# Optimization experiments

Measured on AMD Instinct MI355X. Metric: run time of the kernel, lower is better.

Reference implementation:

```python
import jax, jax.numpy as jnp
import numpy as np

N1, N2, K = 262144, 65536, 16   # dense points, coarse points, knn neighbors
CIN, COUT = 64, 64              # in_planes, out_planes
EPS = 1e-5


def bn(x, g, b, m, v):
    # eval-mode BatchNorm1d with learned affine and running stats
    return (x - m) * jax.lax.rsqrt(v + EPS) * g + b


def setup_inputs() -> dict:
    key = jax.random.key(0)
    ks = jax.random.split(key, 32)
    u = lambda k, *s: jax.random.normal(k, s, jnp.float32)
    lin = lambda k, o, i: jax.random.normal(k, (o, i), jnp.float32) / np.float32(np.sqrt(i))
    inp = dict(
        p1=u(ks[0], N1, 3), p2=u(ks[1], N2, 3),
        x1=u(ks[2], N1, COUT), x2=u(ks[3], N2, CIN),
        knn_idx=jax.random.randint(ks[4], (N2, K), 0, N1),
        # linear1: Linear(COUT,COUT) + BN + ReLU
        w1=lin(ks[5], COUT, COUT), b1=0.01 * u(ks[6], COUT),
        g1=jnp.ones(COUT), be1=jnp.zeros(COUT),
        m1=0.1 * u(ks[7], COUT), v1=jax.random.uniform(ks[8], (COUT,), minval=0.5, maxval=1.5),
        # linear2: Linear(CIN,COUT) + BN + ReLU
        w2=lin(ks[9], COUT, CIN), b2=0.01 * u(ks[10], COUT),
        g2=jnp.ones(COUT), be2=jnp.zeros(COUT),
        m2=0.1 * u(ks[11], COUT), v2=jax.random.uniform(ks[12], (COUT,), minval=0.5, maxval=1.5),
        # channel_shrinker: Linear(CIN+3,CIN) + BN + ReLU + Linear(CIN,1)
        ws1=lin(ks[13], CIN, CIN + 3), bs1=0.01 * u(ks[14], CIN),
        gs=jnp.ones(CIN), bes=jnp.zeros(CIN),
        ms=0.1 * u(ks[15], CIN), vs=jax.random.uniform(ks[16], (CIN,), minval=0.5, maxval=1.5),
        ws2=lin(ks[17], 1, CIN), bs2=0.01 * u(ks[18], 1),
    )
    return inp


def reference(p1, p2, x1, x2, knn_idx,
              w1, b1, g1, be1, m1, v1,
              w2, b2, g2, be2, m2, v2,
              ws1, bs1, gs, bes, ms, vs, ws2, bs2):
    idx = knn_idx.reshape(-1)                                   # [M] = [N2*K], indices into p1
    # relative position of each knn neighbor to its coarse query point
    p_r = p1[idx].reshape(N2, K, 3) - p2[:, None, :]            # [N2,K,3]
    x2k = jnp.concatenate(
        [p_r, jnp.broadcast_to(x2[:, None, :], (N2, K, CIN))], axis=-1
    ).reshape(N2 * K, CIN + 3)                                  # [M, CIN+3]
    # channel_shrinker MLP -> scalar logit per (coarse, neighbor) pair
    h = jax.nn.relu(bn(x2k @ ws1.T + bs1, gs, bes, ms, vs))     # [M, CIN]
    logit = (h @ ws2.T + bs2)[:, 0]                             # [M]
    # scatter_softmax over variable in-degree groups keyed by dense point idx
    gmax = jax.lax.stop_gradient(jax.ops.segment_max(logit, idx, num_segments=N1))
    e = jnp.exp(logit - gmax[idx])
    denom = jax.ops.segment_sum(e, idx, num_segments=N1)
    prob = e / denom[idx]                                       # [M]
    # linear2(x2), broadcast over K neighbors, weight, scatter-sum to dense points
    up_feat = jax.nn.relu(bn(x2 @ w2.T + b2, g2, be2, m2, v2))  # [N2, COUT]
    weighted = (up_feat[:, None, :] * prob.reshape(N2, K, 1)).reshape(N2 * K, COUT)
    up = jax.ops.segment_sum(weighted, idx, num_segments=N1)    # [N1, COUT]
    # skip branch: linear1(x1)
    y1 = jax.nn.relu(bn(x1 @ w1.T + b1, g1, be1, m1, v1))       # [N1, COUT]
    return y1 + up
```

## Files before the change

kernel.cpp:

```cpp
#include <hip/hip_runtime.h>

#define CN1 262144
#define CN2 65536
#define CK  16
#define CM  (CN2*CK)

typedef unsigned short u16;
typedef unsigned int   u32;
typedef float f32x4 __attribute__((ext_vector_type(4)));

__device__ __forceinline__ float b2f(u16 h) {
    union { u32 u; float f; } v; v.u = ((u32)h) << 16; return v.f;
}
__device__ __forceinline__ u16 f2b(float f) {
    union { float f; u32 u; } v; v.f = f;
    u32 lsb = (v.u >> 16) & 1u;
    return (u16)((v.u + 0x7FFFu + lsb) >> 16);
}
__device__ __forceinline__ float u2f(u32 u) {
    union { u32 u; float f; } v; v.u = u; return v.f;
}
__device__ __forceinline__ u32 f2u(float f) {
    union { float f; u32 u; } v; v.f = f; return v.u;
}

#define W_POS   0
#define W_FT    256
#define W_AS    12544
#define W_BS    12608
#define W_WS2   12672
#define W_A2    12736
#define W_B2    12800
#define W_A1    12864
#define W_B1    12928
#define W_BS2   12992
#define W_MODE  13000
#define W_W1T   13056
#define W_W2T   17152
#define W_JP    21248

__device__ __forceinline__ float ldv(const void* p, size_t i, int bf) {
    return bf ? b2f(((const u16*)p)[i]) : ((const float*)p)[i];
}

#define FMA4(A, Wv) \
    (A).x = fmaf(xv_, (Wv).x, (A).x); (A).y = fmaf(xv_, (Wv).y, (A).y); \
    (A).z = fmaf(xv_, (Wv).z, (A).z); (A).w = fmaf(xv_, (Wv).w, (A).w);

#define DECL_ACC16 \
    f32x4 A0={0,0,0,0},A1={0,0,0,0},A2={0,0,0,0},A3={0,0,0,0}, \
          A4={0,0,0,0},A5={0,0,0,0},A6={0,0,0,0},A7={0,0,0,0}, \
          A8={0,0,0,0},A9={0,0,0,0},A10={0,0,0,0},A11={0,0,0,0}, \
          A12={0,0,0,0},A13={0,0,0,0},A14={0,0,0,0},A15={0,0,0,0};

#define WSTEP16(wt, ivar, xval) { \
    float xv_ = (xval); \
    const f32x4* wr_ = (const f32x4*)((wt) + ((size_t)(ivar) << 6)); \
    FMA4(A0, wr_[0])   FMA4(A1, wr_[1])   FMA4(A2, wr_[2])   FMA4(A3, wr_[3]) \
    FMA4(A4, wr_[4])   FMA4(A5, wr_[5])   FMA4(A6, wr_[6])   FMA4(A7, wr_[7]) \
    FMA4(A8, wr_[8])   FMA4(A9, wr_[9])   FMA4(A10,wr_[10])  FMA4(A11,wr_[11]) \
    FMA4(A12,wr_[12])  FMA4(A13,wr_[13])  FMA4(A14,wr_[14])  FMA4(A15,wr_[15]) }

#define GEMV64T(bf, xrow_f, xrow_u4, wt) \
    if (bf) { \
        const uint4* xu_ = (xrow_u4); \
        _Pragma("unroll 2") \
        for (int ii_ = 0; ii_ < 8; ++ii_) { \
            uint4 xc_ = xu_[ii_]; \
            WSTEP16(wt, ii_*8+0, b2f((u16)(xc_.x & 0xffffu))) \
            WSTEP16(wt, ii_*8+1, b2f((u16)(xc_.x >> 16))) \
            WSTEP16(wt, ii_*8+2, b2f((u16)(xc_.y & 0xffffu))) \
            WSTEP16(wt, ii_*8+3, b2f((u16)(xc_.y >> 16))) \
            WSTEP16(wt, ii_*8+4, b2f((u16)(xc_.z & 0xffffu))) \
            WSTEP16(wt, ii_*8+5, b2f((u16)(xc_.z >> 16))) \
            WSTEP16(wt, ii_*8+6, b2f((u16)(xc_.w & 0xffffu))) \
            WSTEP16(wt, ii_*8+7, b2f((u16)(xc_.w >> 16))) \
        } \
    } else { \
        const float4* xf_ = (xrow_f); \
        _Pragma("unroll 2") \
        for (int ii_ = 0; ii_ < 8; ++ii_) { \
            float4 xa_ = xf_[2*ii_], xb_ = xf_[2*ii_+1]; \
            WSTEP16(wt, ii_*8+0, xa_.x) WSTEP16(wt, ii_*8+1, xa_.y) \
            WSTEP16(wt, ii_*8+2, xa_.z) WSTEP16(wt, ii_*8+3, xa_.w) \
            WSTEP16(wt, ii_*8+4, xb_.x) WSTEP16(wt, ii_*8+5, xb_.y) \
            WSTEP16(wt, ii_*8+6, xb_.z) WSTEP16(wt, ii_*8+7, xb_.w) \
        } \
    }

#define DECL_ACC8 \
    f32x4 A0={0,0,0,0},A1={0,0,0,0},A2={0,0,0,0},A3={0,0,0,0}, \
          A4={0,0,0,0},A5={0,0,0,0},A6={0,0,0,0},A7={0,0,0,0};

#define WSTEP8(wtco, ivar, xval) { \
    float xv_ = (xval); \
    const f32x4* wr_ = (const f32x4*)((wtco) + ((size_t)(ivar) << 6)); \
    FMA4(A0, wr_[0])  FMA4(A1, wr_[1])  FMA4(A2, wr_[2])  FMA4(A3, wr_[3]) \
    FMA4(A4, wr_[4])  FMA4(A5, wr_[5])  FMA4(A6, wr_[6])  FMA4(A7, wr_[7]) }

#define GEMV32T(bf, xrow_f, xrow_u4, wtco) \
    if (bf) { \
        const uint4* xu_ = (xrow_u4); \
        _Pragma("unroll 2") \
        for (int ii_ = 0; ii_ < 8; ++ii_) { \
            uint4 xc_ = xu_[ii_]; \
            WSTEP8(wtco, ii_*8+0, b2f((u16)(xc_.x & 0xffffu))) \
            WSTEP8(wtco, ii_*8+1, b2f((u16)(xc_.x >> 16))) \
            WSTEP8(wtco, ii_*8+2, b2f((u16)(xc_.y & 0xffffu))) \
            WSTEP8(wtco, ii_*8+3, b2f((u16)(xc_.y >> 16))) \
            WSTEP8(wtco, ii_*8+4, b2f((u16)(xc_.z & 0xffffu))) \
            WSTEP8(wtco, ii_*8+5, b2f((u16)(xc_.z >> 16))) \
            WSTEP8(wtco, ii_*8+6, b2f((u16)(xc_.w & 0xffffu))) \
            WSTEP8(wtco, ii_*8+7, b2f((u16)(xc_.w >> 16))) \
        } \
    } else { \
        const float4* xf_ = (xrow_f); \
        _Pragma("unroll 2") \
        for (int ii_ = 0; ii_ < 8; ++ii_) { \
            float4 xa_ = xf_[2*ii_], xb_ = xf_[2*ii_+1]; \
            WSTEP8(wtco, ii_*8+0, xa_.x) WSTEP8(wtco, ii_*8+1, xa_.y) \
            WSTEP8(wtco, ii_*8+2, xa_.z) WSTEP8(wtco, ii_*8+3, xa_.w) \
            WSTEP8(wtco, ii_*8+4, xb_.x) WSTEP8(wtco, ii_*8+5, xb_.y) \
            WSTEP8(wtco, ii_*8+6, xb_.z) WSTEP8(wtco, ii_*8+7, xb_.w) \
        } \
    }

#define BNR1(A, av, bv) \
    (A).x = fmaxf(fmaf((A).x,(av).x,(bv).x),0.f); \
    (A).y = fmaxf(fmaf((A).y,(av).y,(bv).y),0.f); \
    (A).z = fmaxf(fmaf((A).z,(av).z,(bv).z),0.f); \
    (A).w = fmaxf(fmaf((A).w,(av).w,(bv).w),0.f);
#define BNR16(aBase, bBase) { \
    const f32x4* av_ = (const f32x4*)(aBase); \
    const f32x4* bv_ = (const f32x4*)(bBase); \
    BNR1(A0,av_[0],bv_[0])   BNR1(A1,av_[1],bv_[1]) \
    BNR1(A2,av_[2],bv_[2])   BNR1(A3,av_[3],bv_[3]) \
    BNR1(A4,av_[4],bv_[4])   BNR1(A5,av_[5],bv_[5]) \
    BNR1(A6,av_[6],bv_[6])   BNR1(A7,av_[7],bv_[7]) \
    BNR1(A8,av_[8],bv_[8])   BNR1(A9,av_[9],bv_[9]) \
    BNR1(A10,av_[10],bv_[10]) BNR1(A11,av_[11],bv_[11]) \
    BNR1(A12,av_[12],bv_[12]) BNR1(A13,av_[13],bv_[13]) \
    BNR1(A14,av_[14],bv_[14]) BNR1(A15,av_[15],bv_[15]) }
#define BNR8(aBase, bBase) { \
    const f32x4* av_ = (const f32x4*)(aBase); \
    const f32x4* bv_ = (const f32x4*)(bBase); \
    BNR1(A0,av_[0],bv_[0]) BNR1(A1,av_[1],bv_[1]) \
    BNR1(A2,av_[2],bv_[2]) BNR1(A3,av_[3],bv_[3]) \
    BNR1(A4,av_[4],bv_[4]) BNR1(A5,av_[5],bv_[5]) \
    BNR1(A6,av_[6],bv_[6]) BNR1(A7,av_[7],bv_[7]) }

#define UFQ(q, AL, AH) { uint4 u_ = ufr_[q]; \
    (AL).x = fmaf(pe_, b2f((u16)(u_.x & 0xffffu)), (AL).x); \
    (AL).y = fmaf(pe_, b2f((u16)(u_.x >> 16)),     (AL).y); \
    (AL).z = fmaf(pe_, b2f((u16)(u_.y & 0xffffu)), (AL).z); \
    (AL).w = fmaf(pe_, b2f((u16)(u_.y >> 16)),     (AL).w); \
    (AH).x = fmaf(pe_, b2f((u16)(u_.z & 0xffffu)), (AH).x); \
    (AH).y = fmaf(pe_, b2f((u16)(u_.z >> 16)),     (AH).y); \
    (AH).z = fmaf(pe_, b2f((u16)(u_.w & 0xffffu)), (AH).z); \
    (AH).w = fmaf(pe_, b2f((u16)(u_.w >> 16)),     (AH).w); }

#define STQ(q, AL, AH, dst) { uint4 o_; \
    o_.x = (u32)f2b((AL).x) | ((u32)f2b((AL).y) << 16); \
    o_.y = (u32)f2b((AL).z) | ((u32)f2b((AL).w) << 16); \
    o_.z = (u32)f2b((AH).x) | ((u32)f2b((AH).y) << 16); \
    o_.w = (u32)f2b((AH).z) | ((u32)f2b((AH).w) << 16); \
    ((uint4*)(dst))[q] = o_; }
#define STORE_BF16V(dst) \
    STQ(0,A0,A1,dst)  STQ(1,A2,A3,dst)  STQ(2,A4,A5,dst)  STQ(3,A6,A7,dst) \
    STQ(4,A8,A9,dst)  STQ(5,A10,A11,dst) STQ(6,A12,A13,dst) STQ(7,A14,A15,dst)
#define STORE_F3216(dst) { f32x4* ov_ = (f32x4*)(dst); \
    ov_[0]=A0;  ov_[1]=A1;  ov_[2]=A2;  ov_[3]=A3; \
    ov_[4]=A4;  ov_[5]=A5;  ov_[6]=A6;  ov_[7]=A7; \
    ov_[8]=A8;  ov_[9]=A9;  ov_[10]=A10;ov_[11]=A11; \
    ov_[12]=A12;ov_[13]=A13;ov_[14]=A14;ov_[15]=A15; }
#define STORE_BF8V(dst) \
    STQ(0,A0,A1,dst) STQ(1,A2,A3,dst) STQ(2,A4,A5,dst) STQ(3,A6,A7,dst)
#define STORE_F328(dst) { f32x4* ov_ = (f32x4*)(dst); \
    ov_[0]=A0; ov_[1]=A1; ov_[2]=A2; ov_[3]=A3; \
    ov_[4]=A4; ov_[5]=A5; ov_[6]=A6; ov_[7]=A7; }

__global__ __launch_bounds__(256) void k_prep(
    const void* __restrict__ w1,  const void* __restrict__ b1,  const void* __restrict__ g1,
    const void* __restrict__ be1, const void* __restrict__ m1,  const void* __restrict__ v1,
    const void* __restrict__ w2,  const void* __restrict__ b2,  const void* __restrict__ g2,
    const void* __restrict__ be2, const void* __restrict__ m2,  const void* __restrict__ v2,
    const void* __restrict__ ws1, const void* __restrict__ bs1, const void* __restrict__ gs,
    const void* __restrict__ bes, const void* __restrict__ ms,  const void* __restrict__ vs,
    const void* __restrict__ ws2, const void* __restrict__ bs2, float* __restrict__ wb,
    u32* __restrict__ offsets, u32* __restrict__ cursor)
{
    int b = blockIdx.x;
    int tid = threadIdx.x;
    if (b > 0) {
        offsets[(b - 1) * 256 + tid] = 0u;
        if (b == 1 && tid == 0) *cursor = 0u;
        return;
    }

    u32 w0 = ((const u32*)g1)[0];
    int bf = (w0 != 0x3F800000u) ? 1 : 0;

    for (int t = tid; t < 64*64; t += 256) {
        int i = t >> 6, c = t & 63;
        wb[W_FT  + t] = ldv(ws1, (size_t)c*67 + 3 + i, bf);
        wb[W_W1T + t] = ldv(w1,  (size_t)c*64 + i, bf);
        wb[W_W2T + t] = ldv(w2,  (size_t)c*64 + i, bf);
    }
    for (int t = tid; t < 64*3; t += 256) {
        int j = t / 3, k = t % 3;
        wb[W_POS + t] = ldv(ws1, (size_t)j*67 + k, bf);
    }
    if (tid < 64) {
        float as = ldv(gs, tid, bf) * rsqrtf(ldv(vs, tid, bf) + 1e-5f);
        float bs = (ldv(bs1, tid, bf) - ldv(ms, tid, bf)) * as + ldv(bes, tid, bf);
        float wc = ldv(ws2, tid, bf);
        wb[W_AS + tid] = as;
        wb[W_BS + tid] = bs;
        wb[W_WS2 + tid] = wc;
        float a2 = ldv(g2, tid, bf) * rsqrtf(ldv(v2, tid, bf) + 1e-5f);
        wb[W_A2 + tid] = a2;
        wb[W_B2 + tid] = (ldv(b2, tid, bf) - ldv(m2, tid, bf)) * a2 + ldv(be2, tid, bf);
        float a1 = ldv(g1, tid, bf) * rsqrtf(ldv(v1, tid, bf) + 1e-5f);
        wb[W_A1 + tid] = a1;
        wb[W_B1 + tid] = (ldv(b1, tid, bf) - ldv(m1, tid, bf)) * a1 + ldv(be1, tid, bf);
        wb[W_JP + tid*8 + 0] = ldv(ws1, (size_t)tid*67 + 0, bf);
        wb[W_JP + tid*8 + 1] = ldv(ws1, (size_t)tid*67 + 1, bf);
        wb[W_JP + tid*8 + 2] = ldv(ws1, (size_t)tid*67 + 2, bf);
        wb[W_JP + tid*8 + 3] = as;
        wb[W_JP + tid*8 + 4] = bs;
        wb[W_JP + tid*8 + 5] = wc;
        wb[W_JP + tid*8 + 6] = 0.f;
        wb[W_JP + tid*8 + 7] = 0.f;
    }
    if (tid == 0) {
        wb[W_BS2] = ldv(bs2, 0, bf);
        ((u32*)wb)[W_MODE] = (u32)bf;
    }
}

__global__ __launch_bounds__(256, 8) void k_coarse2(
    const void* __restrict__ x2, const int* __restrict__ knn,
    const float* __restrict__ wb,
    float* __restrict__ dots, u16* __restrict__ upfeat,
    u32* __restrict__ offsets)
{
    int bf   = (int)((const u32*)wb)[W_MODE];
    int tid  = threadIdx.x;
    int role = blockIdx.x & 1;
    int lane = tid & 63;
    int co   = __builtin_amdgcn_readfirstlane(((tid >> 6) & 1) << 5);
    int n2   = (blockIdx.x >> 1) * 128 + (tid >> 7) * 64 + lane;
    const float4* xf = (const float4*)((const float*)x2 + (size_t)n2 * 64);
    const uint4*  xu = (const uint4*)((const u16*)x2 + (size_t)n2 * 64);

    if (role == 0) {
        if (co == 0) {
            const int4* kv = (const int4*)(knn + (size_t)n2 * 16);
            #pragma unroll
            for (int q = 0; q < 4; q++) {
                int4 t = kv[q];
                atomicAdd(&offsets[t.x & (CN1-1)], 1u);
                atomicAdd(&offsets[t.y & (CN1-1)], 1u);
                atomicAdd(&offsets[t.z & (CN1-1)], 1u);
                atomicAdd(&offsets[t.w & (CN1-1)], 1u);
            }
        }
        DECL_ACC8
        GEMV32T(bf, xf, xu, wb + W_FT + co)
        STORE_F328(dots + (size_t)n2 * 64 + co)
    } else {
        DECL_ACC8
        GEMV32T(bf, xf, xu, wb + W_W2T + co)
        BNR8(wb + W_A2 + co, wb + W_B2 + co)
        STORE_BF8V(upfeat + (size_t)n2 * 64 + co)
    }
}

__global__ __launch_bounds__(256) void k_scan(
    u32* __restrict__ offsets, u32* __restrict__ cursor)
{
    __shared__ u32 s[256];
    __shared__ u32 base;
    int t = threadIdx.x;
    int i = blockIdx.x * 256 + t;
    u32 v = offsets[i];
    s[t] = v; __syncthreads();
    for (int off = 1; off < 256; off <<= 1) {
        u32 add = (t >= off) ? s[t-off] : 0u;
        __syncthreads();
        s[t] += add;
        __syncthreads();
    }
    u32 inc = s[t];
    if (t == 255) base = atomicAdd(cursor, inc);
    __syncthreads();
    offsets[i] = (base + inc - v) << 6;
}

#define LSTEP(j, dv) { f32x4 pa_ = jp[2*(j)], pb_ = jp[2*(j)+1]; \
    float pre_ = fmaf(prz, pa_.z, fmaf(pry, pa_.y, fmaf(prx, pa_.x, (dv)))); \
    float h_ = fmaxf(fmaf(pre_, pa_.w, pb_.x), 0.f); \
    lg = fmaf(h_, pb_.y, lg); }

__global__ __launch_bounds__(256) void k_logit_scatter(
    const void* __restrict__ p1, const void* __restrict__ p2,
    const int* __restrict__ knn, const float* __restrict__ wb,
    const float* __restrict__ dots,
    uint2* __restrict__ epair, u32* __restrict__ offsets)
{
    int bf = (int)((const u32*)wb)[W_MODE];
    int m  = blockIdx.x * 256 + threadIdx.x;
    int n2 = m >> 4;

    int idx = knn[m] & (CN1-1);

    u32 v = atomicAdd(&offsets[idx], 1u);
    u32 pos = ((v >> 6) + (v & 63u)) & (CM-1);

    float prx = ldv(p1, (size_t)idx*3+0, bf) - ldv(p2, (size_t)n2*3+0, bf);
    float pry = ldv(p1, (size_t)idx*3+1, bf) - ldv(p2, (size_t)n2*3+1, bf);
    float prz = ldv(p1, (size_t)idx*3+2, bf) - ldv(p2, (size_t)n2*3+2, bf);

    const f32x4*  jp  = (const f32x4*)(wb + W_JP);
    const float4* dr4 = (const float4*)(dots + (size_t)n2 * 64);
    float lg = 0.f;
    #pragma unroll 4
    for (int jq = 0; jq < 16; ++jq) {
        float4 d4 = dr4[jq];
        LSTEP(jq*4+0, d4.x) LSTEP(jq*4+1, d4.y)
        LSTEP(jq*4+2, d4.z) LSTEP(jq*4+3, d4.w)
    }
    uint2 e;
    e.x = (u32)m;
    e.y = f2u(lg + wb[W_BS2]);
    epair[pos] = e;
}

__global__ __launch_bounds__(256, 4) void k_dense(
    const void* __restrict__ x1, const float* __restrict__ wb,
    const uint2* __restrict__ epair, const u16* __restrict__ upfeat,
    const u32* __restrict__ offsets, void* __restrict__ out)
{
    int bf = (int)((const u32*)wb)[W_MODE];
    int n1 = blockIdx.x * 256 + threadIdx.x;

    u32 pk = offsets[n1];
    int d = (int)(pk & 63u);
    int start = (int)(pk >> 6);

    float mxv = -3.0e38f, s = 0.f;
    for (int e = 0; e < d; ++e) {
        float l = u2f(epair[(u32)(start + e) & (CM-1)].y);
        float mnew = fmaxf(mxv, l);
        s = fmaf(s, __expf(mxv - mnew), __expf(l - mnew));
        mxv = mnew;
    }
    float inv = (d > 0) ? (1.f / s) : 0.f;

    DECL_ACC16
    GEMV64T(bf, (const float4*)((const float*)x1 + (size_t)n1 * 64),
                (const uint4*)((const u16*)x1 + (size_t)n1 * 64),
                wb + W_W1T)
    BNR16(wb + W_A1, wb + W_B1)

    for (int e = 0; e < d; ++e) {
        uint2 t = epair[(u32)(start + e) & (CM-1)];
        float pe_ = __expf(u2f(t.y) - mxv) * inv;
        u32 m = t.x & (CM-1);
        const uint4* ufr_ = (const uint4*)(upfeat + (size_t)(m >> 4) * 64);
        UFQ(0,A0,A1)   UFQ(1,A2,A3)   UFQ(2,A4,A5)   UFQ(3,A6,A7)
        UFQ(4,A8,A9)   UFQ(5,A10,A11) UFQ(6,A12,A13) UFQ(7,A14,A15)
    }

    if (bf) { u16* orow = (u16*)out + (size_t)n1 * 64; STORE_BF16V(orow) }
    else    { STORE_F3216((float*)out + (size_t)n1 * 64) }
}

extern "C" void kernel_launch(void* const* d_in, const int* in_sizes, int n_in,
                              void* d_out, int out_size, void* d_ws, size_t ws_size,
                              hipStream_t stream)
{
    (void)in_sizes; (void)n_in; (void)out_size; (void)ws_size;
    const void* p1   = d_in[0];
    const void* p2   = d_in[1];
    const void* x1   = d_in[2];
    const void* x2   = d_in[3];
    const int*  knn  = (const int*)d_in[4];
    const void* w1   = d_in[5];
    const void* b1   = d_in[6];
    const void* g1   = d_in[7];
    const void* be1  = d_in[8];
    const void* m1   = d_in[9];
    const void* v1   = d_in[10];
    const void* w2   = d_in[11];
    const void* b2   = d_in[12];
    const void* g2   = d_in[13];
    const void* be2  = d_in[14];
    const void* m2   = d_in[15];
    const void* v2   = d_in[16];
    const void* ws1  = d_in[17];
    const void* bs1  = d_in[18];
    const void* gs   = d_in[19];
    const void* bes  = d_in[20];
    const void* ms   = d_in[21];
    const void* vs   = d_in[22];
    const void* ws2w = d_in[23];
    const void* bs2  = d_in[24];

    char* ws = (char*)d_ws;
    float* wb      = (float*)(ws);
    uint2* epair   = (uint2*)(ws + ((size_t)1  << 20));
    u16*   upfeat  = (u16*)  (ws + ((size_t)9  << 20));
    u32*   offsets = (u32*)  (ws + ((size_t)17 << 20));
    u32*   cursor  = (u32*)  (ws + ((size_t)18 << 20));
    float* dots    = (float*)d_out;

    k_prep          <<<1 + CN1/256, 256, 0, stream>>>(w1,b1,g1,be1,m1,v1,
                                                      w2,b2,g2,be2,m2,v2,
                                                      ws1,bs1,gs,bes,ms,vs,
                                                      ws2w, bs2, wb, offsets, cursor);
    k_coarse2       <<<2*(CN2/128), 256, 0, stream>>>(x2, knn, wb, dots, upfeat, offsets);
    k_scan          <<<CN1/256,     256, 0, stream>>>(offsets, cursor);
    k_logit_scatter <<<CM/256,      256, 0, stream>>>(p1, p2, knn, wb, dots,
                                                      epair, offsets);
    k_dense         <<<CN1/256,     256, 0, stream>>>(x1, wb, epair, upfeat,
                                                      offsets, d_out);
}
```

Before: 206.5 us.

## Record per-edge rank during counting to drop scatter atomics; batch two gathers

The counting pass now keeps the value returned by each atomicAdd as a per-edge rank byte. The scatter kernel uses that byte plus the scanned offset, so it no longer needs a second round of atomics on the offsets array. The scan keeps the degree in the low bits as before. In the dense kernel, the gather loop is unrolled by two so both neighbours' upfeat loads are in flight together. This costs an extra 1 MB byte array, and it assumes the in-degree fits in 6 bits, which the code already assumed.

```diff
diff --git a/kernel.cpp b/kernel.cpp
--- a/kernel.cpp
+++ b/kernel.cpp
@@ -6,6 +6,7 @@
 #define CM  (CN2*CK)
 
 typedef unsigned short u16;
+typedef unsigned char  u8;
 typedef unsigned int   u32;
 typedef float f32x4 __attribute__((ext_vector_type(4)));
 
@@ -149,15 +150,15 @@
     BNR1(A4,av_[4],bv_[4]) BNR1(A5,av_[5],bv_[5]) \
     BNR1(A6,av_[6],bv_[6]) BNR1(A7,av_[7],bv_[7]) }
 
-#define UFQ(q, AL, AH) { uint4 u_ = ufr_[q]; \
-    (AL).x = fmaf(pe_, b2f((u16)(u_.x & 0xffffu)), (AL).x); \
-    (AL).y = fmaf(pe_, b2f((u16)(u_.x >> 16)),     (AL).y); \
-    (AL).z = fmaf(pe_, b2f((u16)(u_.y & 0xffffu)), (AL).z); \
-    (AL).w = fmaf(pe_, b2f((u16)(u_.y >> 16)),     (AL).w); \
-    (AH).x = fmaf(pe_, b2f((u16)(u_.z & 0xffffu)), (AH).x); \
-    (AH).y = fmaf(pe_, b2f((u16)(u_.z >> 16)),     (AH).y); \
-    (AH).z = fmaf(pe_, b2f((u16)(u_.w & 0xffffu)), (AH).z); \
-    (AH).w = fmaf(pe_, b2f((u16)(u_.w >> 16)),     (AH).w); }
+#define UFR(u_, AL, AH) { \
+    (AL).x = fmaf(pe_, b2f((u16)((u_).x & 0xffffu)), (AL).x); \
+    (AL).y = fmaf(pe_, b2f((u16)((u_).x >> 16)),     (AL).y); \
+    (AL).z = fmaf(pe_, b2f((u16)((u_).y & 0xffffu)), (AL).z); \
+    (AL).w = fmaf(pe_, b2f((u16)((u_).y >> 16)),     (AL).w); \
+    (AH).x = fmaf(pe_, b2f((u16)((u_).z & 0xffffu)), (AH).x); \
+    (AH).y = fmaf(pe_, b2f((u16)((u_).z >> 16)),     (AH).y); \
+    (AH).z = fmaf(pe_, b2f((u16)((u_).w & 0xffffu)), (AH).z); \
+    (AH).w = fmaf(pe_, b2f((u16)((u_).w >> 16)),     (AH).w); }
 
 #define STQ(q, AL, AH, dst) { uint4 o_; \
     o_.x = (u32)f2b((AL).x) | ((u32)f2b((AL).y) << 16); \
@@ -242,7 +243,7 @@
     const void* __restrict__ x2, const int* __restrict__ knn,
     const float* __restrict__ wb,
     float* __restrict__ dots, u16* __restrict__ upfeat,
-    u32* __restrict__ offsets)
+    u32* __restrict__ offsets, u8* __restrict__ rank8)
 {
     int bf   = (int)((const u32*)wb)[W_MODE];
     int tid  = threadIdx.x;
@@ -256,14 +257,21 @@
     if (role == 0) {
         if (co == 0) {
             const int4* kv = (const int4*)(knn + (size_t)n2 * 16);
-            #pragma unroll
-            for (int q = 0; q < 4; q++) {
-                int4 t = kv[q];
-                atomicAdd(&offsets[t.x & (CN1-1)], 1u);
-                atomicAdd(&offsets[t.y & (CN1-1)], 1u);
-                atomicAdd(&offsets[t.z & (CN1-1)], 1u);
-                atomicAdd(&offsets[t.w & (CN1-1)], 1u);
-            }
+            u32 rw0, rw1, rw2, rw3;
+            #define CNT4(T, RW) { \
+                u32 r0_ = atomicAdd(&offsets[(T).x & (CN1-1)], 1u); \
+                u32 r1_ = atomicAdd(&offsets[(T).y & (CN1-1)], 1u); \
+                u32 r2_ = atomicAdd(&offsets[(T).z & (CN1-1)], 1u); \
+                u32 r3_ = atomicAdd(&offsets[(T).w & (CN1-1)], 1u); \
+                RW = (r0_ & 0xffu) | ((r1_ & 0xffu) << 8) | \
+                     ((r2_ & 0xffu) << 16) | ((r3_ & 0xffu) << 24); }
+            int4 t0 = kv[0]; CNT4(t0, rw0)
+            int4 t1 = kv[1]; CNT4(t1, rw1)
+            int4 t2 = kv[2]; CNT4(t2, rw2)
+            int4 t3 = kv[3]; CNT4(t3, rw3)
+            #undef CNT4
+            uint4 rv; rv.x = rw0; rv.y = rw1; rv.z = rw2; rv.w = rw3;
+            ((uint4*)rank8)[n2] = rv;
         }
         DECL_ACC8
         GEMV32T(bf, xf, xu, wb + W_FT + co)
@@ -294,7 +302,7 @@
     u32 inc = s[t];
     if (t == 255) base = atomicAdd(cursor, inc);
     __syncthreads();
-    offsets[i] = (base + inc - v) << 6;
+    offsets[i] = ((base + inc - v) << 6) | (v & 63u);
 }
 
 #define LSTEP(j, dv) { f32x4 pa_ = jp[2*(j)], pb_ = jp[2*(j)+1]; \
@@ -305,17 +313,16 @@
 __global__ __launch_bounds__(256) void k_logit_scatter(
     const void* __restrict__ p1, const void* __restrict__ p2,
     const int* __restrict__ knn, const float* __restrict__ wb,
-    const float* __restrict__ dots,
-    uint2* __restrict__ epair, u32* __restrict__ offsets)
+    const float* __restrict__ dots, const u8* __restrict__ rank8,
+    const u32* __restrict__ offsets, uint2* __restrict__ epair)
 {
     int bf = (int)((const u32*)wb)[W_MODE];
     int m  = blockIdx.x * 256 + threadIdx.x;
     int n2 = m >> 4;
 
     int idx = knn[m] & (CN1-1);
-
-    u32 v = atomicAdd(&offsets[idx], 1u);
-    u32 pos = ((v >> 6) + (v & 63u)) & (CM-1);
+    u32 rk  = (u32)rank8[m];
+    u32 pos = ((offsets[idx] >> 6) + rk) & (CM-1);
 
     float prx = ldv(p1, (size_t)idx*3+0, bf) - ldv(p2, (size_t)n2*3+0, bf);
     float pry = ldv(p1, (size_t)idx*3+1, bf) - ldv(p2, (size_t)n2*3+1, bf);
@@ -363,13 +370,31 @@
                 wb + W_W1T)
     BNR16(wb + W_A1, wb + W_B1)
 
-    for (int e = 0; e < d; ++e) {
+    int e = 0;
+    for (; e + 2 <= d; e += 2) {
+        uint2 t0 = epair[(u32)(start + e)     & (CM-1)];
+        uint2 t1 = epair[(u32)(start + e + 1) & (CM-1)];
+        const uint4* ua = (const uint4*)(upfeat + (size_t)((t0.x & (CM-1)) >> 4) * 64);
+        const uint4* ub = (const uint4*)(upfeat + (size_t)((t1.x & (CM-1)) >> 4) * 64);
+        uint4 a0 = ua[0], a1 = ua[1], a2 = ua[2], a3 = ua[3];
+        uint4 b0 = ub[0], b1 = ub[1], b2 = ub[2], b3 = ub[3];
+        float p0 = __expf(u2f(t0.y) - mxv) * inv;
+        float p1 = __expf(u2f(t1.y) - mxv) * inv;
+        { float pe_ = p0; UFR(a0,A0,A1) UFR(a1,A2,A3) UFR(a2,A4,A5) UFR(a3,A6,A7) }
+        uint4 a4 = ua[4], a5 = ua[5], a6 = ua[6], a7 = ua[7];
+        uint4 b4 = ub[4], b5 = ub[5], b6 = ub[6], b7 = ub[7];
+        { float pe_ = p1; UFR(b0,A0,A1) UFR(b1,A2,A3) UFR(b2,A4,A5) UFR(b3,A6,A7) }
+        { float pe_ = p0; UFR(a4,A8,A9) UFR(a5,A10,A11) UFR(a6,A12,A13) UFR(a7,A14,A15) }
+        { float pe_ = p1; UFR(b4,A8,A9) UFR(b5,A10,A11) UFR(b6,A12,A13) UFR(b7,A14,A15) }
+    }
+    for (; e < d; ++e) {
         uint2 t = epair[(u32)(start + e) & (CM-1)];
         float pe_ = __expf(u2f(t.y) - mxv) * inv;
-        u32 m = t.x & (CM-1);
-        const uint4* ufr_ = (const uint4*)(upfeat + (size_t)(m >> 4) * 64);
-        UFQ(0,A0,A1)   UFQ(1,A2,A3)   UFQ(2,A4,A5)   UFQ(3,A6,A7)
-        UFQ(4,A8,A9)   UFQ(5,A10,A11) UFQ(6,A12,A13) UFQ(7,A14,A15)
+        const uint4* ufr_ = (const uint4*)(upfeat + (size_t)((t.x & (CM-1)) >> 4) * 64);
+        uint4 c0 = ufr_[0], c1 = ufr_[1], c2 = ufr_[2], c3 = ufr_[3];
+        uint4 c4 = ufr_[4], c5 = ufr_[5], c6 = ufr_[6], c7 = ufr_[7];
+        UFR(c0,A0,A1) UFR(c1,A2,A3) UFR(c2,A4,A5) UFR(c3,A6,A7)
+        UFR(c4,A8,A9) UFR(c5,A10,A11) UFR(c6,A12,A13) UFR(c7,A14,A15)
     }
 
     if (bf) { u16* orow = (u16*)out + (size_t)n1 * 64; STORE_BF16V(orow) }
@@ -413,16 +438,18 @@
     u16*   upfeat  = (u16*)  (ws + ((size_t)9  << 20));
     u32*   offsets = (u32*)  (ws + ((size_t)17 << 20));
     u32*   cursor  = (u32*)  (ws + ((size_t)18 << 20));
+    u8*    rank8   = (u8*)   (ws + ((size_t)19 << 20));
     float* dots    = (float*)d_out;
 
     k_prep          <<<1 + CN1/256, 256, 0, stream>>>(w1,b1,g1,be1,m1,v1,
                                                       w2,b2,g2,be2,m2,v2,
                                                       ws1,bs1,gs,bes,ms,vs,
                                                       ws2w, bs2, wb, offsets, cursor);
-    k_coarse2       <<<2*(CN2/128), 256, 0, stream>>>(x2, knn, wb, dots, upfeat, offsets);
+    k_coarse2       <<<2*(CN2/128), 256, 0, stream>>>(x2, knn, wb, dots, upfeat,
+                                                      offsets, rank8);
     k_scan          <<<CN1/256,     256, 0, stream>>>(offsets, cursor);
     k_logit_scatter <<<CM/256,      256, 0, stream>>>(p1, p2, knn, wb, dots,
-                                                      epair, offsets);
+                                                      rank8, offsets, epair);
     k_dense         <<<CN1/256,     256, 0, stream>>>(x1, wb, epair, upfeat,
                                                       offsets, d_out);
 }
```

Result: slower. 227.1 us (+10.0%).
